# Kernel optimization log

Hardware: AMD Instinct MI355X
Metric: run time of the kernel (lower is better)

## Reference

```python
import jax, jax.numpy as jnp
import numpy as np

I = 256   # input_size
H = 256   # hidden_size
B = 64
T = 2048


def setup_inputs() -> dict:
    key = jax.random.key(0)
    ks = jax.random.split(key, 7)
    s_i = 1.0 / np.sqrt(I)
    s_h = 1.0 / np.sqrt(H)
    return {
        "x": jax.random.normal(ks[0], (B, T, I), dtype=jnp.float32),
        "h0": jax.random.normal(ks[1], (1, B, H), dtype=jnp.float32),
        "c0": jax.random.normal(ks[2], (1, B, H), dtype=jnp.float32),
        # Only l_fi / l_fh affect the output in the original forward (all four
        # gates are computed from the same pre-activation due to a source bug).
        "W_fi": jax.random.uniform(ks[3], (H, I), jnp.float32, -s_i, s_i),
        "b_fi": jax.random.uniform(ks[4], (H,), jnp.float32, -s_i, s_i),
        "W_fh": jax.random.uniform(ks[5], (H, H), jnp.float32, -s_h, s_h),
        "b_fh": jax.random.uniform(ks[6], (H,), jnp.float32, -s_h, s_h),
    }


def reference(x, h0, c0, W_fi, b_fi, W_fh, b_fh):
    # Faithful to the buggy torch source:
    #   f = i = o = sigmoid(l_fi(x_t) + l_fh(ht_1)); m = tanh(same)
    #   ht_1, ct_1 are NEVER updated -> no recurrence; vectorize over time.
    ht_1 = h0[0]  # (B, H), state[0].squeeze(0)
    ct_1 = c0[0]  # (B, H)
    gx = jnp.einsum('bti,hi->bth', x, W_fi) + b_fi          # (B, T, H)
    gh = ht_1 @ W_fh.T + b_fh                               # (B, H)
    g = gx + gh[:, None, :]                                 # (B, T, H)
    s = jax.nn.sigmoid(g)
    m = jnp.tanh(g)
    c = s * ct_1[:, None, :] + s * m                        # c_t per step
    h = s * jnp.tanh(c)                                     # h_t per step
    hidden_seq = jnp.transpose(h, (1, 0, 2))                # (T, B, H), cat dim=0
    return (hidden_seq, (h[:, -1, :], c[:, -1, :]))
```

## Files before the change

### kernel.cpp

```cpp
#include <hip/hip_runtime.h>
#include <hip/hip_bf16.h>
#include <stdint.h>

#define T_SZ 2048
#define B_SZ 64
#define H_SZ 256
#define I_SZ 256
#define M_SZ (B_SZ * T_SZ)
#define TBH  (T_SZ * B_SZ * H_SZ)

typedef float f32x4 __attribute__((ext_vector_type(4)));
typedef short s16x8 __attribute__((ext_vector_type(8)));

__device__ __forceinline__ unsigned pack_bf16(float a, float b) {
    unsigned ua = __float_as_uint(a);
    unsigned ub = __float_as_uint(b);
    ua += 0x7fffu + ((ua >> 16) & 1u);
    ub += 0x7fffu + ((ub >> 16) & 1u);
    return (ua >> 16) | (ub & 0xffff0000u);
}

__global__ void prep_kernel(const float* __restrict__ h0,
                            const float* __restrict__ W_fi,
                            const float* __restrict__ b_fi,
                            const float* __restrict__ W_fh,
                            const float* __restrict__ b_fh,
                            unsigned short* __restrict__ Wb,
                            float* __restrict__ gb) {
    __shared__ float h0s[H_SZ];
    const int b = blockIdx.x;
    const int h = threadIdx.x;
    h0s[h] = h0[b * H_SZ + h];
    __syncthreads();
    const float4* w4 = (const float4*)(W_fh + (size_t)h * H_SZ);
    float acc = 0.f;
#pragma unroll 8
    for (int j = 0; j < H_SZ / 4; ++j) {
        float4 w = w4[j];
        acc = fmaf(w.x, h0s[4 * j + 0], acc);
        acc = fmaf(w.y, h0s[4 * j + 1], acc);
        acc = fmaf(w.z, h0s[4 * j + 2], acc);
        acc = fmaf(w.w, h0s[4 * j + 3], acc);
    }
    gb[b * H_SZ + h] = acc + b_fi[h] + b_fh[h];

    const int e = (b * 256 + h) * 4;
    float4 wv = *(const float4*)(W_fi + e);
    uint2 pk;
    pk.x = pack_bf16(wv.x, wv.y);
    pk.y = pack_bf16(wv.z, wv.w);
    *(uint2*)(Wb + e) = pk;
}

__global__ __launch_bounds__(256, 3) void lstm_main(
    const float* __restrict__ x,
    const unsigned short* __restrict__ Wb,
    const float* __restrict__ gb,
    const float* __restrict__ c0,
    float* __restrict__ out) {
    const int tid  = threadIdx.x;
    const int lane = tid & 63;
    const int wid  = tid >> 6;

    const int orig = blockIdx.x;
    const int mt = (orig >> 4) * 8 + (orig & 7);
    const int nt = (orig >> 3) & 1;
    const int m0 = mt * 128, n0 = nt * 128;
    const int wm = (wid & 1) * 64, wn = (wid >> 1) * 64;
    const int fr = lane & 15;
    const int fq = lane >> 4;

    const float* abase = x + (size_t)(m0 + wm + fr) * I_SZ + fq * 8;
    const unsigned short* bbase = Wb + (size_t)(n0 + wn + fr) * I_SZ + fq * 8;

    f32x4 acc[4][4];
#pragma unroll
    for (int mi = 0; mi < 4; ++mi)
#pragma unroll
        for (int ni = 0; ni < 4; ++ni)
            acc[mi][ni] = (f32x4){0.f, 0.f, 0.f, 0.f};

    float4 alo[4], ahi[4];
#pragma unroll
    for (int mi = 0; mi < 4; ++mi) {
        const float4* p = (const float4*)(abase + mi * 16 * I_SZ);
        alo[mi] = p[0];
        ahi[mi] = p[1];
    }

#pragma unroll
    for (int kt = 0; kt < 8; ++kt) {
        s16x8 bf[4];
#pragma unroll
        for (int ni = 0; ni < 4; ++ni)
            bf[ni] = *(const s16x8*)(bbase + ni * 16 * I_SZ + kt * 32);

        s16x8 af[4];
#pragma unroll
        for (int mi = 0; mi < 4; ++mi) {
            union { s16x8 v; __hip_bfloat162 h[4]; } u;
            u.h[0] = __float22bfloat162_rn(make_float2(alo[mi].x, alo[mi].y));
            u.h[1] = __float22bfloat162_rn(make_float2(alo[mi].z, alo[mi].w));
            u.h[2] = __float22bfloat162_rn(make_float2(ahi[mi].x, ahi[mi].y));
            u.h[3] = __float22bfloat162_rn(make_float2(ahi[mi].z, ahi[mi].w));
            af[mi] = u.v;
        }

        if (kt < 7) {
            const int kof = (kt + 1) * 32;
#pragma unroll
            for (int mi = 0; mi < 4; ++mi) {
                const float4* p = (const float4*)(abase + mi * 16 * I_SZ + kof);
                alo[mi] = p[0];
                ahi[mi] = p[1];
            }
        }

#pragma unroll
        for (int mi = 0; mi < 4; ++mi)
#pragma unroll
            for (int ni = 0; ni < 4; ++ni)
                acc[mi][ni] = __builtin_amdgcn_mfma_f32_16x16x32_bf16(
                    af[mi], bf[ni], acc[mi][ni], 0, 0, 0);
    }

    const int coln = n0 + wn + fr;
    const int bb = (m0 + wm) >> 11;
    float gbv[4], c0v[4];
#pragma unroll
    for (int ni = 0; ni < 4; ++ni) {
        gbv[ni] = gb[bb * H_SZ + coln + ni * 16];
        c0v[ni] = c0[bb * H_SZ + coln + ni * 16];
    }
#pragma unroll
    for (int mi = 0; mi < 4; ++mi) {
#pragma unroll
        for (int r = 0; r < 4; ++r) {
            const int Mg = m0 + wm + mi * 16 + fq * 4 + r;
            const int tt = Mg & (T_SZ - 1);
            const int obase = tt * (B_SZ * H_SZ) + bb * H_SZ;
            const bool last = (tt == T_SZ - 1);
#pragma unroll
            for (int ni = 0; ni < 4; ++ni) {
                const int h = coln + ni * 16;
                float g = acc[mi][ni][r] + gbv[ni];
                float gc = fminf(15.f, fmaxf(-15.f, g));
                float e = __expf(-gc);
                float s = __builtin_amdgcn_rcpf(1.f + e);
                float e2 = e * e;
                float m = (1.f - e2) * __builtin_amdgcn_rcpf(1.f + e2);
                float cv = s * (c0v[ni] + m);
                float cc = fminf(15.f, fmaxf(-15.f, cv));
                float ec = __expf(-2.f * cc);
                float th = (1.f - ec) * __builtin_amdgcn_rcpf(1.f + ec);
                float hv = s * th;
                out[obase + h] = hv;
                if (last) {
                    out[TBH + bb * H_SZ + h] = hv;
                    out[TBH + B_SZ * H_SZ + bb * H_SZ + h] = cv;
                }
            }
        }
    }
}

extern "C" void kernel_launch(void* const* d_in, const int* in_sizes, int n_in,
                              void* d_out, int out_size, void* d_ws, size_t ws_size,
                              hipStream_t stream) {
    const float* x    = (const float*)d_in[0];
    const float* h0   = (const float*)d_in[1];
    const float* c0   = (const float*)d_in[2];
    const float* W_fi = (const float*)d_in[3];
    const float* b_fi = (const float*)d_in[4];
    const float* W_fh = (const float*)d_in[5];
    const float* b_fh = (const float*)d_in[6];
    float* out = (float*)d_out;

    unsigned short* Wb = (unsigned short*)d_ws;
    float* gb = (float*)((char*)d_ws + 131072);

    hipLaunchKernelGGL(prep_kernel, dim3(B_SZ), dim3(H_SZ), 0, stream,
                       h0, W_fi, b_fi, W_fh, b_fh, Wb, gb);
    hipLaunchKernelGGL(lstm_main, dim3(M_SZ / 128 * 2), dim3(256), 0, stream,
                       x, Wb, gb, c0, out);
}
```

Before: 318.0 us.

## Stage A and B tiles through LDS with 64x256 block tiles

The main GEMM kernel now uses 512-thread blocks, each computing a 64-row by full-256-column tile, so x is read once rather than twice across the N split. A and W tiles are cooperatively loaded from global memory, A is converted to bf16, and both are written into padded shared memory with register double-buffering of the next K slice. Barriers separate the LDS writes from the MFMA fragment reads, and setprio is raised around the MFMAs. This removes the redundant global reads of x and the per-wave strided loads, at the cost of two barriers per K step and a smaller per-wave tile (32x64).

Measured after the change: 283.1 us. 11.0% less time.

```diff
diff --git a/kernel.cpp b/kernel.cpp
--- a/kernel.cpp
+++ b/kernel.cpp
@@ -52,80 +52,92 @@
     *(uint2*)(Wb + e) = pk;
 }
 
-__global__ __launch_bounds__(256, 3) void lstm_main(
+__global__ __launch_bounds__(512, 4) void lstm_main(
     const float* __restrict__ x,
     const unsigned short* __restrict__ Wb,
     const float* __restrict__ gb,
     const float* __restrict__ c0,
     float* __restrict__ out) {
+    __shared__ __align__(16) unsigned short As[64 * 40];
+    __shared__ __align__(16) unsigned short Bs[256 * 40];
+
     const int tid  = threadIdx.x;
     const int lane = tid & 63;
     const int wid  = tid >> 6;
-
-    const int orig = blockIdx.x;
-    const int mt = (orig >> 4) * 8 + (orig & 7);
-    const int nt = (orig >> 3) & 1;
-    const int m0 = mt * 128, n0 = nt * 128;
-    const int wm = (wid & 1) * 64, wn = (wid >> 1) * 64;
+    const int m0 = blockIdx.x * 64;
+    const int wm = (wid & 1) * 32;
+    const int wn = (wid >> 1) * 64;
     const int fr = lane & 15;
     const int fq = lane >> 4;
 
-    const float* abase = x + (size_t)(m0 + wm + fr) * I_SZ + fq * 8;
-    const unsigned short* bbase = Wb + (size_t)(n0 + wn + fr) * I_SZ + fq * 8;
+    const int ar  = tid >> 3, ak  = (tid & 7) * 4;
+    const int b0r = tid >> 2, b0k = (tid & 3) * 8;
+    const int b1r = (tid + 512) >> 2, b1k = ((tid + 512) & 3) * 8;
 
-    f32x4 acc[4][4];
+    const float*          aG  = x  + (size_t)(m0 + ar) * I_SZ + ak;
+    const unsigned short* b0G = Wb + b0r * 256 + b0k;
+    const unsigned short* b1G = Wb + b1r * 256 + b1k;
+    unsigned short* aL  = As + ar * 40 + ak;
+    unsigned short* b0L = Bs + b0r * 40 + b0k;
+    unsigned short* b1L = Bs + b1r * 40 + b1k;
+
+    const unsigned short* aF = As + (wm + fr) * 40 + fq * 8;
+    const unsigned short* bF = Bs + (wn + fr) * 40 + fq * 8;
+
+    f32x4 acc[2][4];
 #pragma unroll
-    for (int mi = 0; mi < 4; ++mi)
+    for (int mi = 0; mi < 2; ++mi)
 #pragma unroll
         for (int ni = 0; ni < 4; ++ni)
             acc[mi][ni] = (f32x4){0.f, 0.f, 0.f, 0.f};
 
-    float4 alo[4], ahi[4];
-#pragma unroll
-    for (int mi = 0; mi < 4; ++mi) {
-        const float4* p = (const float4*)(abase + mi * 16 * I_SZ);
-        alo[mi] = p[0];
-        ahi[mi] = p[1];
-    }
+    float4 aw[2];
+    uint4  bw0[2], bw1[2];
+    aw[0]  = *(const float4*)aG;
+    bw0[0] = *(const uint4*)b0G;
+    bw1[0] = *(const uint4*)b1G;
 
 #pragma unroll
     for (int kt = 0; kt < 8; ++kt) {
-        s16x8 bf[4];
+        if (kt < 7) {
+            aw[(kt + 1) & 1]  = *(const float4*)(aG + (kt + 1) * 32);
+            bw0[(kt + 1) & 1] = *(const uint4*)(b0G + (kt + 1) * 32);
+            bw1[(kt + 1) & 1] = *(const uint4*)(b1G + (kt + 1) * 32);
+        }
+        uint2 ap;
+        ap.x = pack_bf16(aw[kt & 1].x, aw[kt & 1].y);
+        ap.y = pack_bf16(aw[kt & 1].z, aw[kt & 1].w);
+        if (kt) {
+            __builtin_amdgcn_sched_barrier(0);
+            __builtin_amdgcn_s_barrier();
+            __builtin_amdgcn_sched_barrier(0);
+        }
+        *(uint2*)aL  = ap;
+        *(uint4*)b0L = bw0[kt & 1];
+        *(uint4*)b1L = bw1[kt & 1];
+        asm volatile("s_waitcnt lgkmcnt(0)" ::: "memory");
+        __builtin_amdgcn_sched_barrier(0);
+        __builtin_amdgcn_s_barrier();
+        __builtin_amdgcn_sched_barrier(0);
+        s16x8 af[2], bf[4];
+#pragma unroll
+        for (int mi = 0; mi < 2; ++mi)
+            af[mi] = *(const s16x8*)(aF + mi * 16 * 40);
 #pragma unroll
         for (int ni = 0; ni < 4; ++ni)
-            bf[ni] = *(const s16x8*)(bbase + ni * 16 * I_SZ + kt * 32);
-
-        s16x8 af[4];
+            bf[ni] = *(const s16x8*)(bF + ni * 16 * 40);
+        __builtin_amdgcn_s_setprio(1);
 #pragma unroll
-        for (int mi = 0; mi < 4; ++mi) {
-            union { s16x8 v; __hip_bfloat162 h[4]; } u;
-            u.h[0] = __float22bfloat162_rn(make_float2(alo[mi].x, alo[mi].y));
-            u.h[1] = __float22bfloat162_rn(make_float2(alo[mi].z, alo[mi].w));
-            u.h[2] = __float22bfloat162_rn(make_float2(ahi[mi].x, ahi[mi].y));
-            u.h[3] = __float22bfloat162_rn(make_float2(ahi[mi].z, ahi[mi].w));
-            af[mi] = u.v;
-        }
-
-        if (kt < 7) {
-            const int kof = (kt + 1) * 32;
-#pragma unroll
-            for (int mi = 0; mi < 4; ++mi) {
-                const float4* p = (const float4*)(abase + mi * 16 * I_SZ + kof);
-                alo[mi] = p[0];
-                ahi[mi] = p[1];
-            }
-        }
-
-#pragma unroll
-        for (int mi = 0; mi < 4; ++mi)
+        for (int mi = 0; mi < 2; ++mi)
 #pragma unroll
             for (int ni = 0; ni < 4; ++ni)
                 acc[mi][ni] = __builtin_amdgcn_mfma_f32_16x16x32_bf16(
                     af[mi], bf[ni], acc[mi][ni], 0, 0, 0);
+        __builtin_amdgcn_s_setprio(0);
     }
 
-    const int coln = n0 + wn + fr;
-    const int bb = (m0 + wm) >> 11;
+    const int bb = m0 >> 11;
+    const int coln = wn + fr;
     float gbv[4], c0v[4];
 #pragma unroll
     for (int ni = 0; ni < 4; ++ni) {
@@ -133,7 +145,7 @@
         c0v[ni] = c0[bb * H_SZ + coln + ni * 16];
     }
 #pragma unroll
-    for (int mi = 0; mi < 4; ++mi) {
+    for (int mi = 0; mi < 2; ++mi) {
 #pragma unroll
         for (int r = 0; r < 4; ++r) {
             const int Mg = m0 + wm + mi * 16 + fq * 4 + r;
@@ -181,6 +193,6 @@
 
     hipLaunchKernelGGL(prep_kernel, dim3(B_SZ), dim3(H_SZ), 0, stream,
                        h0, W_fi, b_fi, W_fh, b_fh, Wb, gb);
-    hipLaunchKernelGGL(lstm_main, dim3(M_SZ / 128 * 2), dim3(256), 0, stream,
+    hipLaunchKernelGGL(lstm_main, dim3(M_SZ / 64), dim3(512), 0, stream,
                        x, Wb, gb, c0, out);
 }
```
